# Performance work log

Measured on AMD Instinct MI355X. Metric: run time of the kernel, lower is better.

Reference implementation:

```python
import jax, jax.numpy as jnp
import numpy as np

B, S, D = 4, 4096, 2048
SCAN, STATE = 128, 16


def setup_inputs() -> dict:
    key = jax.random.key(0)
    ks = jax.random.split(key, 8)
    scale = 1.0 / np.sqrt(D)
    scale_s = 1.0 / np.sqrt(SCAN)
    x = jax.random.normal(ks[0], (B, S, D), dtype=jnp.float32)
    Wi = jax.random.normal(ks[1], (SCAN, D), dtype=jnp.float32) * scale
    Wo = jax.random.normal(ks[2], (D, SCAN), dtype=jnp.float32) * 0.02  # torch zero-inits; small random for nontrivial output
    A_log = jax.random.normal(ks[3], (SCAN, STATE), dtype=jnp.float32) * 0.1
    Wb = jax.random.normal(ks[4], (STATE, SCAN), dtype=jnp.float32) * scale_s
    Wc = jax.random.normal(ks[5], (STATE, SCAN), dtype=jnp.float32) * scale_s
    Wdt = jax.random.normal(ks[6], (SCAN, SCAN), dtype=jnp.float32) * scale_s
    b_dt = jnp.full((SCAN,), -3.0, dtype=jnp.float32)
    Wg = jax.random.normal(ks[7], (SCAN, D), dtype=jnp.float32) * scale
    return {"x": x, "Wi": Wi, "Wo": Wo, "A_log": A_log, "Wb": Wb,
            "Wc": Wc, "Wdt": Wdt, "b_dt": b_dt, "Wg": Wg}


def _selective_scan_ffn(x, Wi, Wo, A_log, Wb, Wc, Wdt, b_dt, Wg):
    z = jnp.einsum('bsd,nd->bsn', x, Wi)                      # [B,S,SCAN]
    gate = jax.nn.silu(jnp.einsum('bsd,nd->bsn', x, Wg))      # [B,S,SCAN]
    A = -jnp.exp(A_log)                                        # [SCAN,STATE]
    B_in = jnp.einsum('bsn,kn->bsk', z, Wb)                   # [B,S,STATE]
    C_in = jnp.einsum('bsn,kn->bsk', z, Wc)                   # [B,S,STATE]
    dt = jax.nn.softplus(jnp.einsum('bsn,mn->bsm', z, Wdt) + b_dt)  # [B,S,SCAN]
    A_bar = 1.0 + dt[..., None] * A                            # [B,S,SCAN,STATE]

    def step(state, inp):
        a_t, dt_t, z_t, b_t, c_t = inp
        # state: [B,SCAN,STATE]
        state = a_t * state + dt_t[..., None] * (z_t[..., None] * b_t[:, None, :])
        y = jnp.einsum('bnk,bk->bn', state, c_t)               # [B,SCAN]
        return state, y

    xs = (jnp.moveaxis(A_bar, 1, 0), jnp.moveaxis(dt, 1, 0),
          jnp.moveaxis(z, 1, 0), jnp.moveaxis(B_in, 1, 0), jnp.moveaxis(C_in, 1, 0))
    state0 = jnp.zeros((x.shape[0], Wi.shape[0], A_log.shape[1]), dtype=x.dtype)
    _, ys = jax.lax.scan(step, state0, xs)                     # [S,B,SCAN]
    y = jnp.moveaxis(ys, 0, 1) * gate                          # [B,S,SCAN]
    return jnp.einsum('bsn,dn->bsd', y, Wo)                    # [B,S,D]


def reference(x, Wi, Wo, A_log, Wb, Wc, Wdt, b_dt, Wg):
    return _selective_scan_ffn(x, Wi, Wo, A_log, Wb, Wc, Wdt, b_dt, Wg)
```

## Files before the change

kernel.cpp:

```cpp
#include <hip/hip_runtime.h>
#include <hip/hip_bf16.h>
#include <math.h>

using bf16 = __hip_bfloat16;
typedef __attribute__((ext_vector_type(8))) short bf16x8;
typedef __attribute__((ext_vector_type(8))) short short8;
typedef __attribute__((ext_vector_type(4))) float f32x4;

#define AS1 __attribute__((address_space(1)))
#define AS3 __attribute__((address_space(3)))

constexpr int BATCH = 4;
constexpr int SEQ   = 4096;
constexpr int DIM   = 2048;
constexpr int SCAN  = 128;
constexpr int STATE = 16;
constexpr int LCH   = 16;
constexpr int NCH   = SEQ / LCH;

__device__ __forceinline__ float bf2f(bf16 v) { return __bfloat162float(v); }
__device__ __forceinline__ bf16  f2bf(float v) { return __float2bfloat16(v); }
__device__ __forceinline__ float bfbits(unsigned short u) {
  return __uint_as_float((unsigned)u << 16);
}

__device__ __forceinline__ int probe_dtype(const unsigned short* __restrict__ xp) {
  int cnt = 0;
#pragma unroll
  for (int i = 0; i < 64; ++i) {
    int e = (xp[i] >> 7) & 0xFF;
    cnt += (e >= 107 && e <= 147) ? 1 : 0;
  }
  return (cnt >= 51) ? 1 : 0;
}

__device__ __forceinline__ void conv_b(const void* src, bf16* dst, int n, int f,
                                       int gtid, int nt) {
  if (f) { const bf16* s = (const bf16*)src;  for (int i = gtid; i < n; i += nt) dst[i] = s[i]; }
  else   { const float* s = (const float*)src; for (int i = gtid; i < n; i += nt) dst[i] = f2bf(s[i]); }
}
__device__ __forceinline__ void conv_f(const void* src, float* dst, int n, int f,
                                       int gtid, int nt) {
  if (f) { const bf16* s = (const bf16*)src;  for (int i = gtid; i < n; i += nt) dst[i] = bf2f(s[i]); }
  else   { const float* s = (const float*)src; for (int i = gtid; i < n; i += nt) dst[i] = s[i]; }
}
__device__ __forceinline__ void conv_aneg(const void* src, float* dst, int n, int f,
                                          int gtid, int nt) {
  if (f) { const bf16* s = (const bf16*)src;  for (int i = gtid; i < n; i += nt) dst[i] = -expf(bf2f(s[i])); }
  else   { const float* s = (const float*)src; for (int i = gtid; i < n; i += nt) dst[i] = -expf(s[i]); }
}

__global__ __launch_bounds__(256) void kconv_w(
    const unsigned short* __restrict__ xprobe,
    const void* Wi, const void* Wg, const void* Wo, const void* Wdt,
    const void* Wb, const void* Wc, const void* bdt, const void* Alog,
    bf16* Wzg, bf16* Wob, bf16* Wdtb, bf16* Wbb, bf16* Wcb,
    float* bdtf, float* Anegf, int* __restrict__ flag) {
  int f = probe_dtype(xprobe);
  if (blockIdx.x == 0 && threadIdx.x == 0) *flag = f;
  int nt = gridDim.x * blockDim.x;
  int g  = blockIdx.x * blockDim.x + threadIdx.x;
  conv_b(Wi,  Wzg,               SCAN * DIM,  f, g, nt);
  conv_b(Wg,  Wzg + SCAN * DIM,  SCAN * DIM,  f, g, nt);
  conv_b(Wo,  Wob,  DIM * SCAN,  f, g, nt);
  conv_b(Wdt, Wdtb, SCAN * SCAN, f, g, nt);
  conv_b(Wb,  Wbb,  STATE * SCAN, f, g, nt);
  conv_b(Wc,  Wcb,  STATE * SCAN, f, g, nt);
  conv_f(bdt,  bdtf,  SCAN,          f, g, nt);
  conv_aneg(Alog, Anegf, SCAN * STATE, f, g, nt);
}

__device__ __forceinline__ int swzb(int row, int colbyte) {
  return row * 128 + (colbyte ^ ((row & 7) << 4));
}

struct ARegs { float4 v; };

template <int F>
__device__ __forceinline__ ARegs loadA(const void* __restrict__ xin, size_t rowbase,
                                       int k0, int ae) {
  ARegs r;
  if (F) {
    float2 t = *(const float2*)((const bf16*)xin + rowbase + k0 + ae);
    r.v.x = t.x; r.v.y = t.y; r.v.z = 0.f; r.v.w = 0.f;
  } else {
    r.v = *(const float4*)((const float*)xin + rowbase + k0 + ae);
  }
  return r;
}

template <int F>
__device__ __forceinline__ void writeA(char* abuf, int ar, int ae, const ARegs& rg) {
  char* d = abuf + swzb(ar, ae * 2);
  if (F) {
    *(float2*)d = make_float2(rg.v.x, rg.v.y);
  } else {
    union { float2 f2; bf16 b[4]; } u;
    u.b[0] = f2bf(rg.v.x); u.b[1] = f2bf(rg.v.y);
    u.b[2] = f2bf(rg.v.z); u.b[3] = f2bf(rg.v.w);
    *(float2*)d = u.f2;
  }
}

__device__ __forceinline__ void stageB(const bf16* __restrict__ W, int k0,
                                       char* bbuf, int tid) {
  int w = tid >> 6;
#pragma unroll
  for (int i = 0; i < 2; ++i) {
    int off = i * 16384 + tid * 16;
    int r   = off >> 7;
    int cbl = off & 127;
    int cbs = cbl ^ ((r & 7) << 4);
    const bf16* src = W + (size_t)r * DIM + k0 + (cbs >> 1);
    char* lb = bbuf + i * 16384 + w * 1024;
    __builtin_amdgcn_global_load_lds((const AS1 void*)src, (AS3 void*)lb, 16, 0, 0);
  }
}

__device__ __forceinline__ void compute64x256_16w(const char* abuf, const char* bbuf,
                                                  int tid, f32x4 acc[2][2]) {
  int l = tid & 63, w = tid >> 6;
  int wr = (w >> 3) * 32;
  int wc = (w & 7) * 32;
  int lr = l & 15, lk = (l >> 4) * 8;
#pragma unroll
  for (int kk = 0; kk < 64; kk += 32) {
    int cb = (kk + lk) * 2;
    bf16x8 a[2], b[2];
#pragma unroll
    for (int m = 0; m < 2; ++m)
      a[m] = *(const bf16x8*)(abuf + swzb(wr + m * 16 + lr, cb));
#pragma unroll
    for (int n = 0; n < 2; ++n)
      b[n] = *(const bf16x8*)(bbuf + swzb(wc + n * 16 + lr, cb));
#pragma unroll
    for (int m = 0; m < 2; ++m)
#pragma unroll
      for (int n = 0; n < 2; ++n)
        acc[m][n] = __builtin_amdgcn_mfma_f32_16x16x32_bf16(a[m], b[n], acc[m][n], 0, 0, 0);
  }
}

__device__ __forceinline__ void vm_wait3() { asm volatile("s_waitcnt vmcnt(3)" ::: "memory"); __builtin_amdgcn_sched_barrier(0); }
__device__ __forceinline__ void vm_wait0() { asm volatile("s_waitcnt vmcnt(0)" ::: "memory"); __builtin_amdgcn_sched_barrier(0); }
__device__ __forceinline__ void lgkm0_barrier() {
  asm volatile("s_waitcnt lgkmcnt(0)" ::: "memory");
  __builtin_amdgcn_sched_barrier(0);
  __builtin_amdgcn_s_barrier();
}

template <int F>
__device__ __forceinline__ void k1_main(const void* __restrict__ xin,
                                        const bf16* __restrict__ W,
                                        char* lds, size_t xrow, int ar, int ae,
                                        int tid, f32x4 acc[2][2]) {
  constexpr int NK = DIM / 64;
  constexpr int BUF = 40960;
  ARegs aH = loadA<F>(xin, xrow, 0, ae);
  stageB(W, 0, lds + 0 * BUF + 8192, tid);
  ARegs aN = loadA<F>(xin, xrow, 64, ae);
  stageB(W, 64, lds + 1 * BUF + 8192, tid);
  vm_wait3();
  writeA<F>(lds + 0 * BUF, ar, ae, aH);
  aH = aN;
  lgkm0_barrier();

  for (int t = 0; t < NK; ++t) {
    char* curb = lds + (t % 3) * BUF;
    if (t + 2 < NK) {
      aN = loadA<F>(xin, xrow, (t + 2) * 64, ae);
      stageB(W, (t + 2) * 64, lds + ((t + 2) % 3) * BUF + 8192, tid);
    }
    compute64x256_16w(curb, curb + 8192, tid, acc);
    if (t + 1 < NK) {
      if (t + 2 < NK) vm_wait3();
      else            vm_wait0();
      writeA<F>(lds + ((t + 1) % 3) * BUF, ar, ae, aH);
      aH = aN;
      lgkm0_barrier();
    }
  }
}

__global__ __launch_bounds__(1024) void k12_zg(const void* __restrict__ xin,
                                               const bf16* __restrict__ Wzg,
                                               const bf16* __restrict__ Wdtb,
                                               const bf16* __restrict__ Wbb,
                                               const bf16* __restrict__ Wcb,
                                               const float* __restrict__ bdtf,
                                               const float* __restrict__ Aneg,
                                               bf16* __restrict__ z,
                                               bf16* __restrict__ gate,
                                               float* __restrict__ dt,
                                               float* __restrict__ Bv,
                                               float* __restrict__ Cv,
                                               float* __restrict__ fin,
                                               float* __restrict__ apr,
                                               const int* __restrict__ flag) {
  __shared__ char lds[122880];
  int tid = threadIdx.x;
  int mb  = blockIdx.x;
  int m0  = mb * 64;
  int f   = *flag;
  int ar  = tid >> 4;
  int ae  = (tid & 15) * 4;
  size_t xrow = ((size_t)m0 + ar) * DIM;

  f32x4 acc[2][2];
#pragma unroll
  for (int m = 0; m < 2; ++m)
#pragma unroll
    for (int n = 0; n < 2; ++n)
#pragma unroll
      for (int j = 0; j < 4; ++j) acc[m][n][j] = 0.f;

  if (f) k1_main<1>(xin, Wzg, lds, xrow, ar, ae, tid, acc);
  else   k1_main<0>(xin, Wzg, lds, xrow, ar, ae, tid, acc);

  __syncthreads();

  bf16 (*zl)[128]   = (bf16 (*)[128])(lds);
  bf16 (*wl)[136]   = (bf16 (*)[136])(lds + 16384);
  bf16 (*dtlb)[128] = (bf16 (*)[128])(lds + 59904);
  bf16 (*Blcb)[16]  = (bf16 (*)[16]) (lds + 76288);

  {
    int l = tid & 63, w = tid >> 6;
    int wr = (w >> 3) * 32;
    int wcg = (w & 7) * 32;
    int sel = wcg >> 7;
    int cb  = wcg & 127;
    int lr = l & 15, lj = (l >> 4) * 4;
    bf16* o = sel ? gate : z;
#pragma unroll
    for (int m = 0; m < 2; ++m)
#pragma unroll
      for (int n = 0; n < 2; ++n)
#pragma unroll
        for (int j = 0; j < 4; ++j) {
          int rowl = wr + m * 16 + lj + j;
          int col  = cb + n * 16 + lr;
          float v = acc[m][n][j];
          if (sel) v = v / (1.f + expf(-v));
          bf16 bv = f2bf(v);
          o[(size_t)(m0 + rowl) * SCAN + col] = bv;
          if (!sel) zl[rowl][col] = bv;
        }
  }
  for (int idx = tid; idx < 160 * 16; idx += 1024) {
    int r = idx >> 4, c8 = (idx & 15) << 3;
    const bf16* src;
    if (r < 128)      src = Wdtb + r * 128;
    else if (r < 144) src = Wbb + (r - 128) * 128;
    else              src = Wcb + (r - 144) * 128;
    *(short8*)&wl[r][c8] = *(const short8*)(src + c8);
  }
  __syncthreads();

  if (tid < 256) {
    int l = tid & 63, w = tid >> 6;
    int lr = l & 15, lk = (l >> 4) * 8, lj = (l >> 4) * 4;
    f32x4 acc2[10];
#pragma unroll
    for (int n = 0; n < 10; ++n)
#pragma unroll
      for (int j = 0; j < 4; ++j) acc2[n][j] = 0.f;

#pragma unroll
    for (int kk = 0; kk < 128; kk += 32) {
      bf16x8 a = *(const bf16x8*)&zl[w * 16 + lr][kk + lk];
#pragma unroll
      for (int n = 0; n < 10; ++n) {
        bf16x8 bfr = *(const bf16x8*)&wl[n * 16 + lr][kk + lk];
        acc2[n] = __builtin_amdgcn_mfma_f32_16x16x32_bf16(a, bfr, acc2[n], 0, 0, 0);
      }
    }

#pragma unroll
    for (int n = 0; n < 10; ++n) {
      int o = n * 16 + lr;
#pragma unroll
      for (int j = 0; j < 4; ++j) {
        int row = w * 16 + lj + j;
        float v = acc2[n][j];
        if (o < 128) {
          v += bdtf[o];
          v = fmaxf(v, 0.f) + log1pf(expf(-fabsf(v)));
          dt[(size_t)(m0 + row) * SCAN + o] = v;
          dtlb[row][o] = f2bf(v);
        } else if (o < 144) {
          Bv[(size_t)(m0 + row) * STATE + (o - 128)] = v;
          Blcb[row][o - 128] = f2bf(v);
        } else {
          Cv[(size_t)(m0 + row) * STATE + (o - 144)] = v;
        }
      }
    }
  }
  __syncthreads();

  if (tid < 512) {
    int n  = tid & 127;
    int cc = tid >> 7;
    int b   = m0 >> 12;
    int ch0 = (m0 & 4095) >> 4;
    float A[STATE];
#pragma unroll
    for (int k = 0; k < STATE; ++k) A[k] = Aneg[n * STATE + k];

    float st[STATE], ap[STATE];
#pragma unroll
    for (int k = 0; k < STATE; ++k) { st[k] = 0.f; ap[k] = 1.f; }
#pragma unroll
    for (int t = 0; t < LCH; ++t) {
      int row = cc * LCH + t;
      float d = bf2f(dtlb[row][n]);
      float u = d * bf2f(zl[row][n]);
#pragma unroll
      for (int kg = 0; kg < 4; ++kg) {
        unsigned long long bb = *(const unsigned long long*)&Blcb[row][kg * 4];
        float b0 = bfbits((unsigned short)bb);
        float b1 = bfbits((unsigned short)(bb >> 16));
        float b2 = bfbits((unsigned short)(bb >> 32));
        float b3 = bfbits((unsigned short)(bb >> 48));
        float a;
        a = fmaf(d, A[kg*4+0], 1.f); st[kg*4+0] = fmaf(a, st[kg*4+0], u * b0); ap[kg*4+0] *= a;
        a = fmaf(d, A[kg*4+1], 1.f); st[kg*4+1] = fmaf(a, st[kg*4+1], u * b1); ap[kg*4+1] *= a;
        a = fmaf(d, A[kg*4+2], 1.f); st[kg*4+2] = fmaf(a, st[kg*4+2], u * b2); ap[kg*4+2] *= a;
        a = fmaf(d, A[kg*4+3], 1.f); st[kg*4+3] = fmaf(a, st[kg*4+3], u * b3); ap[kg*4+3] *= a;
      }
    }
    size_t base = ((size_t)b * NCH + (ch0 + cc)) * (STATE * SCAN) + n;
#pragma unroll
    for (int k = 0; k < STATE; ++k) {
      fin[base + k * SCAN] = st[k];
      apr[base + k * SCAN] = ap[k];
    }
  }
}

__global__ __launch_bounds__(64) void k3b(const float* __restrict__ fin,
                                          float* __restrict__ apr) {
  int c  = blockIdx.x * 64 + threadIdx.x;
  int b  = c >> 11;
  int kn = c & 2047;
  size_t base = (size_t)b * NCH * 2048 + kn;
  float s = 0.f;
  for (int g = 0; g < NCH; g += 16) {
    float fv[16], av[16];
#pragma unroll
    for (int i = 0; i < 16; ++i) {
      size_t o = base + (size_t)(g + i) * 2048;
      fv[i] = fin[o];
      av[i] = apr[o];
    }
#pragma unroll
    for (int i = 0; i < 16; ++i) {
      size_t o = base + (size_t)(g + i) * 2048;
      apr[o] = s;
      s = fmaf(av[i], s, fv[i]);
    }
  }
}

__device__ __forceinline__ int swz256(int row, int colbyte) {
  return row * 256 + (colbyte ^ ((row & 7) << 4));
}

__global__ __launch_bounds__(512) void k34(
    const float* __restrict__ dt, const bf16* __restrict__ z,
    const float* __restrict__ Bv, const float* __restrict__ Cv,
    const float* __restrict__ Aneg, const float* __restrict__ inc,
    const bf16* __restrict__ gate, const bf16* __restrict__ Wob,
    void* __restrict__ outv, const int* __restrict__ flag) {
  __shared__ char lds[25088];
  char*  ygl = lds;
  float (*Bl)[STATE] = (float (*)[STATE])(lds + 16384);
  float (*Cl)[STATE] = (float (*)[STATE])(lds + 20480);
  int tid = threadIdx.x;
  int mb  = blockIdx.x;
  int nb  = blockIdx.y;
  int m0  = mb * 64;

  if (tid < 256)      ((float4*)&Bl[0][0])[tid]       = ((const float4*)(Bv + (size_t)m0 * STATE))[tid];
  else                ((float4*)&Cl[0][0])[tid - 256] = ((const float4*)(Cv + (size_t)m0 * STATE))[tid - 256];

  {
    int n  = tid & 127;
    int cc = tid >> 7;
    int b   = m0 >> 12;
    int ch0 = (m0 & 4095) >> 4;
    size_t base = ((size_t)b * NCH + (ch0 + cc)) * (STATE * SCAN) + n;
    float A[STATE], st[STATE];
#pragma unroll
    for (int k = 0; k < STATE; ++k) {
      A[k]  = Aneg[n * STATE + k];
      st[k] = inc[base + k * SCAN];
    }
    __syncthreads();

    const float* dtp = dt   + ((size_t)m0 + cc * LCH) * SCAN + n;
    const bf16*  zp  = z    + ((size_t)m0 + cc * LCH) * SCAN + n;
    const bf16*  gp  = gate + ((size_t)m0 + cc * LCH) * SCAN + n;
#pragma unroll
    for (int t = 0; t < LCH; ++t) {
      int row = cc * LCH + t;
      float d = dtp[t * SCAN];
      float u = d * bf2f(zp[t * SCAN]);
      float g = bf2f(gp[t * SCAN]);
      float y0 = 0.f, y1 = 0.f, y2 = 0.f, y3 = 0.f;
#pragma unroll
      for (int kg = 0; kg < 4; ++kg) {
        float4 B4 = *(const float4*)&Bl[row][kg * 4];
        float4 C4 = *(const float4*)&Cl[row][kg * 4];
        float a, p = 0.f;
        a = fmaf(d, A[kg*4+0], 1.f); st[kg*4+0] = fmaf(a, st[kg*4+0], u * B4.x); p = fmaf(st[kg*4+0], C4.x, p);
        a = fmaf(d, A[kg*4+1], 1.f); st[kg*4+1] = fmaf(a, st[kg*4+1], u * B4.y); p = fmaf(st[kg*4+1], C4.y, p);
        a = fmaf(d, A[kg*4+2], 1.f); st[kg*4+2] = fmaf(a, st[kg*4+2], u * B4.z); p = fmaf(st[kg*4+2], C4.z, p);
        a = fmaf(d, A[kg*4+3], 1.f); st[kg*4+3] = fmaf(a, st[kg*4+3], u * B4.w); p = fmaf(st[kg*4+3], C4.w, p);
        if (kg == 0) y0 = p; else if (kg == 1) y1 = p; else if (kg == 2) y2 = p; else y3 = p;
      }
      float y = (y0 + y1) + (y2 + y3);
      *(bf16*)(ygl + swz256(row, n * 2)) = f2bf(y * g);
    }
  }
  __syncthreads();

  int l = tid & 63, w = tid >> 6;
  int lr = l & 15, lk = (l >> 4) * 8;
  int f = *flag;
  int colw = nb * 1024 + w * 128;
#pragma unroll
  for (int g2 = 0; g2 < 2; ++g2) {
    int nc0 = colw + g2 * 64;
    f32x4 acc[4][4];
#pragma unroll
    for (int m = 0; m < 4; ++m)
#pragma unroll
      for (int n = 0; n < 4; ++n)
#pragma unroll
        for (int j = 0; j < 4; ++j) acc[m][n][j] = 0.f;

#pragma unroll
    for (int kk = 0; kk < 128; kk += 32) {
      int cb = (kk + lk) * 2;
      bf16x8 a[4], b[4];
#pragma unroll
      for (int m = 0; m < 4; ++m)
        a[m] = *(const bf16x8*)(ygl + swz256(m * 16 + lr, cb));
#pragma unroll
      for (int n = 0; n < 4; ++n)
        b[n] = *(const bf16x8*)(Wob + (size_t)(nc0 + n * 16 + lr) * SCAN + kk + lk);
#pragma unroll
      for (int m = 0; m < 4; ++m)
#pragma unroll
        for (int n = 0; n < 4; ++n)
          acc[m][n] = __builtin_amdgcn_mfma_f32_16x16x32_bf16(a[m], b[n], acc[m][n], 0, 0, 0);
    }

    int lj = (l >> 4) * 4;
#pragma unroll
    for (int m = 0; m < 4; ++m)
#pragma unroll
      for (int n = 0; n < 4; ++n)
#pragma unroll
        for (int j = 0; j < 4; ++j) {
          int row = m0 + m * 16 + lj + j;
          int col = nc0 + n * 16 + lr;
          size_t off = (size_t)row * DIM + col;
          float v = acc[m][n][j];
          if (f) ((bf16*)outv)[off] = f2bf(v);
          else   ((float*)outv)[off] = v;
        }
  }
}

extern "C" void kernel_launch(void* const* d_in, const int* in_sizes, int n_in,
                              void* d_out, int out_size, void* d_ws, size_t ws_size,
                              hipStream_t stream) {
  const void* x     = d_in[0];
  const void* Wi    = d_in[1];
  const void* Wo    = d_in[2];
  const void* A_log = d_in[3];
  const void* Wb    = d_in[4];
  const void* Wc    = d_in[5];
  const void* Wdt   = d_in[6];
  const void* b_dt  = d_in[7];
  const void* Wg    = d_in[8];

  const size_t M = (size_t)BATCH * SEQ;
  char* p = (char*)d_ws;
  int*   flag = (int*)p;    p += 256;
  bf16*  Wzg  = (bf16*)p;   p += (size_t)2 * SCAN * DIM * 2;
  bf16*  Wob  = (bf16*)p;   p += (size_t)DIM * SCAN * 2;
  bf16*  Wdtb = (bf16*)p;   p += (size_t)SCAN * SCAN * 2;
  bf16*  Wbb  = (bf16*)p;   p += (size_t)STATE * SCAN * 2;
  bf16*  Wcb  = (bf16*)p;   p += (size_t)STATE * SCAN * 2;
  float* bdtf = (float*)p;  p += SCAN * 4;
  float* Anegf= (float*)p;  p += (size_t)SCAN * STATE * 4;
  bf16*  z    = (bf16*)p;   p += M * SCAN * 2;
  bf16*  gate = (bf16*)p;   p += M * SCAN * 2;
  float* dt   = (float*)p;  p += M * SCAN * 4;
  float* Bv   = (float*)p;  p += M * STATE * 4;
  float* Cv   = (float*)p;  p += M * STATE * 4;
  float* fin  = (float*)p;  p += (size_t)BATCH * NCH * SCAN * STATE * 4;
  float* apr  = (float*)p;  p += (size_t)BATCH * NCH * SCAN * STATE * 4;

  kconv_w <<<256, 256, 0, stream>>>((const unsigned short*)x,
                                    Wi, Wg, Wo, Wdt, Wb, Wc, b_dt, A_log,
                                    Wzg, Wob, Wdtb, Wbb, Wcb, bdtf, Anegf, flag);
  k12_zg  <<<dim3(256), 1024, 0, stream>>>(x, Wzg, Wdtb, Wbb, Wcb, bdtf, Anegf,
                                           z, gate, dt, Bv, Cv, fin, apr, flag);
  k3b     <<<dim3(128), 64, 0, stream>>>(fin, apr);
  k34     <<<dim3(256, 2), 512, 0, stream>>>(dt, z, Bv, Cv, Anegf, apr, gate,
                                             Wob, d_out, flag);
}
```

Before: 133.7 us.

## Fuse projection, chunk scan, and output GEMM into one cooperative kernel

```diff
diff --git a/kernel.cpp b/kernel.cpp
--- a/kernel.cpp
+++ b/kernel.cpp
@@ -1,6 +1,9 @@
 #include <hip/hip_runtime.h>
 #include <hip/hip_bf16.h>
+#include <hip/hip_cooperative_groups.h>
 #include <math.h>
+
+namespace cg = cooperative_groups;
 
 using bf16 = __hip_bfloat16;
 typedef __attribute__((ext_vector_type(8))) short bf16x8;
@@ -73,6 +76,9 @@
 __device__ __forceinline__ int swzb(int row, int colbyte) {
   return row * 128 + (colbyte ^ ((row & 7) << 4));
 }
+__device__ __forceinline__ int swz256(int row, int colbyte) {
+  return row * 256 + (colbyte ^ ((row & 7) << 4));
+}
 
 struct ARegs { float4 v; };
 
@@ -142,6 +148,7 @@
 }
 
 __device__ __forceinline__ void vm_wait3() { asm volatile("s_waitcnt vmcnt(3)" ::: "memory"); __builtin_amdgcn_sched_barrier(0); }
+__device__ __forceinline__ void vm_wait2() { asm volatile("s_waitcnt vmcnt(2)" ::: "memory"); __builtin_amdgcn_sched_barrier(0); }
 __device__ __forceinline__ void vm_wait0() { asm volatile("s_waitcnt vmcnt(0)" ::: "memory"); __builtin_amdgcn_sched_barrier(0); }
 __device__ __forceinline__ void lgkm0_barrier() {
   asm volatile("s_waitcnt lgkmcnt(0)" ::: "memory");
@@ -182,21 +189,28 @@
   }
 }
 
-__global__ __launch_bounds__(1024) void k12_zg(const void* __restrict__ xin,
-                                               const bf16* __restrict__ Wzg,
-                                               const bf16* __restrict__ Wdtb,
-                                               const bf16* __restrict__ Wbb,
-                                               const bf16* __restrict__ Wcb,
-                                               const float* __restrict__ bdtf,
-                                               const float* __restrict__ Aneg,
-                                               bf16* __restrict__ z,
-                                               bf16* __restrict__ gate,
-                                               float* __restrict__ dt,
-                                               float* __restrict__ Bv,
-                                               float* __restrict__ Cv,
-                                               float* __restrict__ fin,
-                                               float* __restrict__ apr,
-                                               const int* __restrict__ flag) {
+__device__ __forceinline__ void stageWo(const bf16* __restrict__ Wob, int row0,
+                                        char* buf, int tid) {
+  int w = tid >> 6;
+#pragma unroll
+  for (int i = 0; i < 2; ++i) {
+    int off = i * 16384 + tid * 16;
+    int r   = off >> 8;
+    int cbl = off & 255;
+    int cbs = cbl ^ ((r & 7) << 4);
+    const bf16* src = Wob + (size_t)(row0 + r) * SCAN + (cbs >> 1);
+    char* lb = buf + i * 16384 + w * 1024;
+    __builtin_amdgcn_global_load_lds((const AS1 void*)src, (AS3 void*)lb, 16, 0, 0);
+  }
+}
+
+__global__ __launch_bounds__(1024) void kfused(
+    const void* __restrict__ xin, const bf16* __restrict__ Wzg,
+    const bf16* __restrict__ Wdtb, const bf16* __restrict__ Wbb,
+    const bf16* __restrict__ Wcb, const float* __restrict__ bdtf,
+    const float* __restrict__ Aneg, const bf16* __restrict__ Wob,
+    float* __restrict__ fin, float* __restrict__ apr,
+    void* __restrict__ outv, const int* __restrict__ flag) {
   __shared__ char lds[122880];
   int tid = threadIdx.x;
   int mb  = blockIdx.x;
@@ -219,10 +233,13 @@
 
   __syncthreads();
 
-  bf16 (*zl)[128]   = (bf16 (*)[128])(lds);
-  bf16 (*wl)[136]   = (bf16 (*)[136])(lds + 16384);
-  bf16 (*dtlb)[128] = (bf16 (*)[128])(lds + 59904);
-  bf16 (*Blcb)[16]  = (bf16 (*)[16]) (lds + 76288);
+  bf16 (*zl)[128]    = (bf16 (*)[128])(lds);
+  bf16 (*wl)[136]    = (bf16 (*)[136])(lds + 16384);
+  bf16 (*dtlb)[128]  = (bf16 (*)[128])(lds + 59904);
+  bf16 (*Blcb)[16]   = (bf16 (*)[16]) (lds + 76288);
+  bf16 (*Clcb)[16]   = (bf16 (*)[16]) (lds + 78336);
+  bf16 (*gatel)[128] = (bf16 (*)[128])(lds + 80384);
+  char* ygl          = lds + 96768;
 
   {
     int l = tid & 63, w = tid >> 6;
@@ -231,7 +248,6 @@
     int sel = wcg >> 7;
     int cb  = wcg & 127;
     int lr = l & 15, lj = (l >> 4) * 4;
-    bf16* o = sel ? gate : z;
 #pragma unroll
     for (int m = 0; m < 2; ++m)
 #pragma unroll
@@ -241,10 +257,12 @@
           int rowl = wr + m * 16 + lj + j;
           int col  = cb + n * 16 + lr;
           float v = acc[m][n][j];
-          if (sel) v = v / (1.f + expf(-v));
-          bf16 bv = f2bf(v);
-          o[(size_t)(m0 + rowl) * SCAN + col] = bv;
-          if (!sel) zl[rowl][col] = bv;
+          if (sel) {
+            v = v / (1.f + expf(-v));
+            gatel[rowl][col] = f2bf(v);
+          } else {
+            zl[rowl][col] = f2bf(v);
+          }
         }
   }
   for (int idx = tid; idx < 160 * 16; idx += 1024) {
@@ -286,13 +304,11 @@
         if (o < 128) {
           v += bdtf[o];
           v = fmaxf(v, 0.f) + log1pf(expf(-fabsf(v)));
-          dt[(size_t)(m0 + row) * SCAN + o] = v;
           dtlb[row][o] = f2bf(v);
         } else if (o < 144) {
-          Bv[(size_t)(m0 + row) * STATE + (o - 128)] = v;
           Blcb[row][o - 128] = f2bf(v);
         } else {
-          Cv[(size_t)(m0 + row) * STATE + (o - 144)] = v;
+          Clcb[row][o - 144] = f2bf(v);
         }
       }
     }
@@ -337,55 +353,37 @@
       apr[base + k * SCAN] = ap[k];
     }
   }
-}
-
-__global__ __launch_bounds__(64) void k3b(const float* __restrict__ fin,
-                                          float* __restrict__ apr) {
-  int c  = blockIdx.x * 64 + threadIdx.x;
-  int b  = c >> 11;
-  int kn = c & 2047;
-  size_t base = (size_t)b * NCH * 2048 + kn;
-  float s = 0.f;
-  for (int g = 0; g < NCH; g += 16) {
-    float fv[16], av[16];
-#pragma unroll
-    for (int i = 0; i < 16; ++i) {
-      size_t o = base + (size_t)(g + i) * 2048;
-      fv[i] = fin[o];
-      av[i] = apr[o];
-    }
-#pragma unroll
-    for (int i = 0; i < 16; ++i) {
-      size_t o = base + (size_t)(g + i) * 2048;
-      apr[o] = s;
-      s = fmaf(av[i], s, fv[i]);
-    }
-  }
-}
-
-__device__ __forceinline__ int swz256(int row, int colbyte) {
-  return row * 256 + (colbyte ^ ((row & 7) << 4));
-}
-
-__global__ __launch_bounds__(512) void k34(
-    const float* __restrict__ dt, const bf16* __restrict__ z,
-    const float* __restrict__ Bv, const float* __restrict__ Cv,
-    const float* __restrict__ Aneg, const float* __restrict__ inc,
-    const bf16* __restrict__ gate, const bf16* __restrict__ Wob,
-    void* __restrict__ outv, const int* __restrict__ flag) {
-  __shared__ char lds[25088];
-  char*  ygl = lds;
-  float (*Bl)[STATE] = (float (*)[STATE])(lds + 16384);
-  float (*Cl)[STATE] = (float (*)[STATE])(lds + 20480);
-  int tid = threadIdx.x;
-  int mb  = blockIdx.x;
-  int nb  = blockIdx.y;
-  int m0  = mb * 64;
-
-  if (tid < 256)      ((float4*)&Bl[0][0])[tid]       = ((const float4*)(Bv + (size_t)m0 * STATE))[tid];
-  else                ((float4*)&Cl[0][0])[tid - 256] = ((const float4*)(Cv + (size_t)m0 * STATE))[tid - 256];
-
-  {
+
+  __threadfence();
+  cg::this_grid().sync();
+
+  if (mb < 8) {
+    int c  = mb * 1024 + tid;
+    int b  = c >> 11;
+    int kn = c & 2047;
+    size_t base = (size_t)b * NCH * 2048 + kn;
+    float s = 0.f;
+    for (int g = 0; g < NCH; g += 16) {
+      float fv[16], av[16];
+#pragma unroll
+      for (int i = 0; i < 16; ++i) {
+        size_t o = base + (size_t)(g + i) * 2048;
+        fv[i] = fin[o];
+        av[i] = apr[o];
+      }
+#pragma unroll
+      for (int i = 0; i < 16; ++i) {
+        size_t o = base + (size_t)(g + i) * 2048;
+        apr[o] = s;
+        s = fmaf(av[i], s, fv[i]);
+      }
+    }
+  }
+
+  __threadfence();
+  cg::this_grid().sync();
+
+  if (tid < 512) {
     int n  = tid & 127;
     int cc = tid >> 7;
     int b   = m0 >> 12;
@@ -395,29 +393,32 @@
 #pragma unroll
     for (int k = 0; k < STATE; ++k) {
       A[k]  = Aneg[n * STATE + k];
-      st[k] = inc[base + k * SCAN];
-    }
-    __syncthreads();
-
-    const float* dtp = dt   + ((size_t)m0 + cc * LCH) * SCAN + n;
-    const bf16*  zp  = z    + ((size_t)m0 + cc * LCH) * SCAN + n;
-    const bf16*  gp  = gate + ((size_t)m0 + cc * LCH) * SCAN + n;
+      st[k] = apr[base + k * SCAN];
+    }
 #pragma unroll
     for (int t = 0; t < LCH; ++t) {
       int row = cc * LCH + t;
-      float d = dtp[t * SCAN];
-      float u = d * bf2f(zp[t * SCAN]);
-      float g = bf2f(gp[t * SCAN]);
+      float d = bf2f(dtlb[row][n]);
+      float u = d * bf2f(zl[row][n]);
+      float g = bf2f(gatel[row][n]);
       float y0 = 0.f, y1 = 0.f, y2 = 0.f, y3 = 0.f;
 #pragma unroll
       for (int kg = 0; kg < 4; ++kg) {
-        float4 B4 = *(const float4*)&Bl[row][kg * 4];
-        float4 C4 = *(const float4*)&Cl[row][kg * 4];
+        unsigned long long bb = *(const unsigned long long*)&Blcb[row][kg * 4];
+        unsigned long long cbits = *(const unsigned long long*)&Clcb[row][kg * 4];
+        float b0 = bfbits((unsigned short)bb);
+        float b1 = bfbits((unsigned short)(bb >> 16));
+        float b2 = bfbits((unsigned short)(bb >> 32));
+        float b3 = bfbits((unsigned short)(bb >> 48));
+        float c0 = bfbits((unsigned short)cbits);
+        float c1 = bfbits((unsigned short)(cbits >> 16));
+        float c2 = bfbits((unsigned short)(cbits >> 32));
+        float c3 = bfbits((unsigned short)(cbits >> 48));
         float a, p = 0.f;
-        a = fmaf(d, A[kg*4+0], 1.f); st[kg*4+0] = fmaf(a, st[kg*4+0], u * B4.x); p = fmaf(st[kg*4+0], C4.x, p);
-        a = fmaf(d, A[kg*4+1], 1.f); st[kg*4+1] = fmaf(a, st[kg*4+1], u * B4.y); p = fmaf(st[kg*4+1], C4.y, p);
-        a = fmaf(d, A[kg*4+2], 1.f); st[kg*4+2] = fmaf(a, st[kg*4+2], u * B4.z); p = fmaf(st[kg*4+2], C4.z, p);
-        a = fmaf(d, A[kg*4+3], 1.f); st[kg*4+3] = fmaf(a, st[kg*4+3], u * B4.w); p = fmaf(st[kg*4+3], C4.w, p);
+        a = fmaf(d, A[kg*4+0], 1.f); st[kg*4+0] = fmaf(a, st[kg*4+0], u * b0); p = fmaf(st[kg*4+0], c0, p);
+        a = fmaf(d, A[kg*4+1], 1.f); st[kg*4+1] = fmaf(a, st[kg*4+1], u * b1); p = fmaf(st[kg*4+1], c1, p);
+        a = fmaf(d, A[kg*4+2], 1.f); st[kg*4+2] = fmaf(a, st[kg*4+2], u * b2); p = fmaf(st[kg*4+2], c2, p);
+        a = fmaf(d, A[kg*4+3], 1.f); st[kg*4+3] = fmaf(a, st[kg*4+3], u * b3); p = fmaf(st[kg*4+3], c3, p);
         if (kg == 0) y0 = p; else if (kg == 1) y1 = p; else if (kg == 2) y2 = p; else y3 = p;
       }
       float y = (y0 + y1) + (y2 + y3);
@@ -426,52 +427,54 @@
   }
   __syncthreads();
 
-  int l = tid & 63, w = tid >> 6;
-  int lr = l & 15, lk = (l >> 4) * 8;
-  int f = *flag;
-  int colw = nb * 1024 + w * 128;
-#pragma unroll
-  for (int g2 = 0; g2 < 2; ++g2) {
-    int nc0 = colw + g2 * 64;
-    f32x4 acc[4][4];
-#pragma unroll
-    for (int m = 0; m < 4; ++m)
-#pragma unroll
-      for (int n = 0; n < 4; ++n)
-#pragma unroll
-        for (int j = 0; j < 4; ++j) acc[m][n][j] = 0.f;
-
-#pragma unroll
-    for (int kk = 0; kk < 128; kk += 32) {
-      int cb = (kk + lk) * 2;
-      bf16x8 a[4], b[4];
-#pragma unroll
-      for (int m = 0; m < 4; ++m)
-        a[m] = *(const bf16x8*)(ygl + swz256(m * 16 + lr, cb));
-#pragma unroll
-      for (int n = 0; n < 4; ++n)
-        b[n] = *(const bf16x8*)(Wob + (size_t)(nc0 + n * 16 + lr) * SCAN + kk + lk);
-#pragma unroll
-      for (int m = 0; m < 4; ++m)
-#pragma unroll
-        for (int n = 0; n < 4; ++n)
-          acc[m][n] = __builtin_amdgcn_mfma_f32_16x16x32_bf16(a[m], b[n], acc[m][n], 0, 0, 0);
-    }
-
-    int lj = (l >> 4) * 4;
-#pragma unroll
-    for (int m = 0; m < 4; ++m)
-#pragma unroll
-      for (int n = 0; n < 4; ++n)
+  {
+    char* wo0 = lds;
+    char* wo1 = lds + 32768;
+    int l = tid & 63, w = tid >> 6;
+    int lr = l & 15, lk = (l >> 4) * 8, lj = (l >> 4) * 4;
+    int wrr = (w >> 2) * 16;
+    int wcc = (w & 3) * 32;
+
+    stageWo(Wob, 0, wo0, tid);
+    vm_wait0();
+    __builtin_amdgcn_s_barrier();
+
+    for (int nb = 0; nb < 16; ++nb) {
+      char* cur = (nb & 1) ? wo1 : wo0;
+      char* nxt = (nb & 1) ? wo0 : wo1;
+      if (nb + 1 < 16) {
+        stageWo(Wob, (nb + 1) * 128, nxt, tid);
+        vm_wait2();
+      } else {
+        vm_wait0();
+      }
+      __builtin_amdgcn_s_barrier();
+
+      f32x4 a7[2];
+#pragma unroll
+      for (int j = 0; j < 4; ++j) { a7[0][j] = 0.f; a7[1][j] = 0.f; }
+#pragma unroll
+      for (int kk = 0; kk < 128; kk += 32) {
+        int cb = (kk + lk) * 2;
+        bf16x8 av = *(const bf16x8*)(ygl + swz256(wrr + lr, cb));
+        bf16x8 b0 = *(const bf16x8*)(cur + swz256(wcc + lr, cb));
+        bf16x8 b1 = *(const bf16x8*)(cur + swz256(wcc + 16 + lr, cb));
+        a7[0] = __builtin_amdgcn_mfma_f32_16x16x32_bf16(av, b0, a7[0], 0, 0, 0);
+        a7[1] = __builtin_amdgcn_mfma_f32_16x16x32_bf16(av, b1, a7[1], 0, 0, 0);
+      }
+#pragma unroll
+      for (int n = 0; n < 2; ++n)
 #pragma unroll
         for (int j = 0; j < 4; ++j) {
-          int row = m0 + m * 16 + lj + j;
-          int col = nc0 + n * 16 + lr;
+          int row = m0 + wrr + lj + j;
+          int col = nb * 128 + wcc + n * 16 + lr;
           size_t off = (size_t)row * DIM + col;
-          float v = acc[m][n][j];
+          float v = a7[n][j];
           if (f) ((bf16*)outv)[off] = f2bf(v);
           else   ((float*)outv)[off] = v;
         }
+      lgkm0_barrier();
+    }
   }
 }
 
@@ -488,7 +491,6 @@
   const void* b_dt  = d_in[7];
   const void* Wg    = d_in[8];
 
-  const size_t M = (size_t)BATCH * SEQ;
   char* p = (char*)d_ws;
   int*   flag = (int*)p;    p += 256;
   bf16*  Wzg  = (bf16*)p;   p += (size_t)2 * SCAN * DIM * 2;
@@ -498,20 +500,18 @@
   bf16*  Wcb  = (bf16*)p;   p += (size_t)STATE * SCAN * 2;
   float* bdtf = (float*)p;  p += SCAN * 4;
   float* Anegf= (float*)p;  p += (size_t)SCAN * STATE * 4;
-  bf16*  z    = (bf16*)p;   p += M * SCAN * 2;
-  bf16*  gate = (bf16*)p;   p += M * SCAN * 2;
-  float* dt   = (float*)p;  p += M * SCAN * 4;
-  float* Bv   = (float*)p;  p += M * STATE * 4;
-  float* Cv   = (float*)p;  p += M * STATE * 4;
   float* fin  = (float*)p;  p += (size_t)BATCH * NCH * SCAN * STATE * 4;
   float* apr  = (float*)p;  p += (size_t)BATCH * NCH * SCAN * STATE * 4;
 
   kconv_w <<<256, 256, 0, stream>>>((const unsigned short*)x,
                                     Wi, Wg, Wo, Wdt, Wb, Wc, b_dt, A_log,
                                     Wzg, Wob, Wdtb, Wbb, Wcb, bdtf, Anegf, flag);
-  k12_zg  <<<dim3(256), 1024, 0, stream>>>(x, Wzg, Wdtb, Wbb, Wcb, bdtf, Anegf,
-                                           z, gate, dt, Bv, Cv, fin, apr, flag);
-  k3b     <<<dim3(128), 64, 0, stream>>>(fin, apr);
-  k34     <<<dim3(256, 2), 512, 0, stream>>>(dt, z, Bv, Cv, Anegf, apr, gate,
-                                             Wob, d_out, flag);
-}
+
+  void* outp = d_out;
+  const void* xv = x;
+  void* args[] = {(void*)&xv, (void*)&Wzg, (void*)&Wdtb, (void*)&Wbb, (void*)&Wcb,
+                  (void*)&bdtf, (void*)&Anegf, (void*)&Wob, (void*)&fin, (void*)&apr,
+                  (void*)&outp, (void*)&flag};
+  hipLaunchCooperativeKernel((const void*)kfused, dim3(256), dim3(1024),
+                             args, 0, stream);
+}
```

Measured after the change: 358.5 us. +168.2%, slower.
